# Performance work log

Measured on AMD Instinct MI355X. Metric: run time of the kernel, lower is better.

The kernel has to match this reference:

```python
import jax, jax.numpy as jnp
import numpy as np

LN2 = float(np.log(2.0))
N_ATOMS = 100_000
N_PAIRS = 2_000_000
F = 64     # number_of_atom_features
R = 16     # number_of_radial_basis_functions
N_RES = 3


def setup_inputs() -> dict:
    key = jax.random.key(0)
    ks = jax.random.split(key, 16)
    s = 0.05
    inp = {
        "pair_indices": jax.random.randint(ks[0], (2, N_PAIRS), 0, N_ATOMS, dtype=jnp.int32),
        "f_ij": jax.random.normal(ks[1], (N_PAIRS, 1, R), dtype=jnp.float32),
        "d_ij": jax.random.uniform(ks[2], (N_PAIRS, 1), dtype=jnp.float32),
        "atomic_embedding": jax.random.normal(ks[3], (N_ATOMS, F), dtype=jnp.float32),
        # AttentionMask parameter G: [F, R]
        "G": jax.random.normal(ks[4], (F, R), dtype=jnp.float32),
        # interaction_i / interaction_j linear layers (stored as [in, out])
        "Wi": jax.random.normal(ks[5], (F, F), dtype=jnp.float32) * s,
        "bi": jnp.zeros((F,), dtype=jnp.float32),
        "Wj": jax.random.normal(ks[6], (F, F), dtype=jnp.float32) * s,
        "bj": jnp.zeros((F,), dtype=jnp.float32),
        # residual blocks, stacked over N_RES
        "res_W1": jax.random.normal(ks[7], (N_RES, F, F), dtype=jnp.float32) * s,
        "res_b1": jnp.zeros((N_RES, F), dtype=jnp.float32),
        "res_W2": jax.random.normal(ks[8], (N_RES, F, F), dtype=jnp.float32) * s,
        "res_b2": jnp.zeros((N_RES, F), dtype=jnp.float32),
        # process_v linear
        "Wv": jax.random.normal(ks[9], (F, F), dtype=jnp.float32) * s,
        "bv": jnp.zeros((F,), dtype=jnp.float32),
    }
    return inp


def reference(pair_indices, f_ij, d_ij, atomic_embedding,
              G, Wi, bi, Wj, bj, res_W1, res_b1, res_W2, res_b2, Wv, bv):
    idx_i, idx_j = pair_indices[0], pair_indices[1]
    f = f_ij.squeeze(1)                                  # [P, R]

    # ShiftedSoftplus on node embeddings
    x = jax.nn.softplus(atomic_embedding) - LN2          # [N, F]

    x_i_prime = jax.nn.softplus(x @ Wi + bi)             # [N, F]
    x_j_prime = jax.nn.softplus(x[idx_j] @ Wj + bj)      # [P, F] (gather)
    f_prime = f @ G.T                                    # [P, F] attention mask

    msg = x_j_prime * f_prime                            # [P, F]
    summed = jax.ops.segment_sum(msg, idx_i, num_segments=atomic_embedding.shape[0])

    v = x_i_prime + summed                               # [N, F]
    for l in range(res_W1.shape[0]):
        h = jax.nn.softplus(v @ res_W1[l] + res_b1[l])
        v = v + (h @ res_W2[l] + res_b2[l])
    return jax.nn.softplus(v) @ Wv + bv
```

## Files before the change

### kernel.cpp

```cpp
#include <hip/hip_runtime.h>
#include <math.h>

#define FDIM 64
#define RDIM 16
#define LN2F 0.69314718055994530942f
#define LTS 68
#define NBINR 14336
#define NCHUNK 64

typedef __bf16 bf8_t __attribute__((ext_vector_type(8)));
typedef float  f4_t  __attribute__((ext_vector_type(4)));
typedef _Float16 h2_t __attribute__((ext_vector_type(2)));

__device__ __forceinline__ float sp(float x) {
    return fmaxf(x, 0.0f) + __logf(1.0f + __expf(-fabsf(x)));
}

__device__ __forceinline__ float fdot2f(h2_t a, h2_t b, float c) {
#if __has_builtin(__builtin_amdgcn_fdot2)
    return __builtin_amdgcn_fdot2(a, b, c, false);
#else
    return c + (float)a[0] * (float)b[0] + (float)a[1] * (float)b[1];
#endif
}

__global__ __launch_bounds__(256) void k_prep(
    const float* s0, const float* s1, const float* s2, const float* s3,
    const float* s4, const float* s5, const float* s6, const float* s7,
    const float* s8, __bf16* __restrict__ dst)
{
    const float* srcs[9] = {s0, s1, s2, s3, s4, s5, s6, s7, s8};
    const float* W = srcs[blockIdx.x];
    __bf16* d = dst + (size_t)blockIdx.x * 4096;
    for (int slot = threadIdx.x; slot < 512; slot += 256) {
        int f = slot >> 6, l = slot & 63;
        int kt = f >> 2, nt = f & 3;
        int row0 = kt * 32 + (l >> 4) * 8;
        int col = nt * 16 + (l & 15);
#pragma unroll
        for (int j = 0; j < 8; ++j)
            d[slot * 8 + j] = (__bf16)W[(row0 + j) * FDIM + col];
    }
}

__global__ __launch_bounds__(256) void k_hist2(
    const int* __restrict__ idx_i, int* __restrict__ Cmat,
    int P, int N, int nRange)
{
    __shared__ int h[NBINR];
    const int chunk = blockIdx.x / nRange;
    const int range = blockIdx.x % nRange;
    const int lo = range * NBINR;
    const int nb = min(NBINR, N - lo);
    for (int u = threadIdx.x; u < NBINR; u += 256) h[u] = 0;
    __syncthreads();

    const int chunkSz = (P + NCHUNK - 1) / NCHUNK;
    const int cs = chunk * chunkSz;
    const int ce = min(P, cs + chunkSz);
    int p = cs + threadIdx.x;
    for (; p + 768 < ce; p += 1024) {
        int i0 = idx_i[p];
        int i1 = idx_i[p + 256];
        int i2 = idx_i[p + 512];
        int i3 = idx_i[p + 768];
        unsigned u0 = (unsigned)(i0 - lo);
        unsigned u1 = (unsigned)(i1 - lo);
        unsigned u2 = (unsigned)(i2 - lo);
        unsigned u3 = (unsigned)(i3 - lo);
        if (u0 < (unsigned)nb) atomicAdd(&h[u0], 1);
        if (u1 < (unsigned)nb) atomicAdd(&h[u1], 1);
        if (u2 < (unsigned)nb) atomicAdd(&h[u2], 1);
        if (u3 < (unsigned)nb) atomicAdd(&h[u3], 1);
    }
    for (; p < ce; p += 256) {
        unsigned u = (unsigned)(idx_i[p] - lo);
        if (u < (unsigned)nb) atomicAdd(&h[u], 1);
    }
    __syncthreads();
    for (int u = threadIdx.x; u < nb; u += 256)
        Cmat[(size_t)chunk * N + lo + u] = h[u];
}

__global__ __launch_bounds__(256) void k_scanR(
    int* __restrict__ Cmat, int* __restrict__ tot, int N)
{
    const int bA = blockIdx.x * 512 + threadIdx.x;
    const int bB = bA + 256;
    const bool okA = bA < N, okB = bB < N;
    int runA = 0, runB = 0;
    for (int c = 0; c < NCHUNK; ++c) {
        const size_t base = (size_t)c * N;
        if (okA) { int val = Cmat[base + bA]; Cmat[base + bA] = runA; runA += val; }
        if (okB) { int val = Cmat[base + bB]; Cmat[base + bB] = runB; runB += val; }
    }
    if (okA) tot[bA] = runA;
    if (okB) tot[bB] = runB;
}

__device__ __forceinline__ void tile_in(float* T, const float* __restrict__ src,
                                        int a0, int rows, int lane)
{
#pragma unroll 4
    for (int i = 0; i < 16; ++i) {
        int r = i * 4 + (lane >> 4);
        int col = (lane & 15) * 4;
        float4 val = make_float4(0.f, 0.f, 0.f, 0.f);
        if (r < rows) val = *(const float4*)&src[(size_t)(a0 + r) * FDIM + col];
        *(float4*)&T[r * LTS + col] = val;
    }
}

__device__ __forceinline__ void build_a(const float* T, int lane, bool actLn2,
                                        bf8_t (&aF)[4][2])
{
    const int l15 = lane & 15, quad = lane >> 4;
#pragma unroll
    for (int mt = 0; mt < 4; ++mt) {
#pragma unroll
        for (int kt = 0; kt < 2; ++kt) {
            const float* rp = &T[(mt * 16 + l15) * LTS + kt * 32 + quad * 8];
            float4 u0 = *(const float4*)rp;
            float4 u1 = *(const float4*)(rp + 4);
            float e[8] = {u0.x, u0.y, u0.z, u0.w, u1.x, u1.y, u1.z, u1.w};
            bf8_t f;
#pragma unroll
            for (int j = 0; j < 8; ++j) {
                float t = actLn2 ? (sp(e[j]) - LN2F) : e[j];
                f[j] = (__bf16)t;
            }
            aF[mt][kt] = f;
        }
    }
}

__global__ __launch_bounds__(256) void k_atoms(
    const float* __restrict__ emb, const __bf16* __restrict__ wf,
    const float* __restrict__ bi, const float* __restrict__ bj,
    float* __restrict__ v, float* __restrict__ y, int N)
{
    __shared__ float tile[4][64 * LTS];
    const int lane = threadIdx.x & 63;
    const int wv = threadIdx.x >> 6;
    float* T = tile[wv];
    const int l15 = lane & 15, quad = lane >> 4;

    const bf8_t* wiF = (const bf8_t*)wf;
    const bf8_t* wjF = (const bf8_t*)(wf + 4096);
    bf8_t wi[2][4], wj[2][4];
#pragma unroll
    for (int kt = 0; kt < 2; ++kt)
#pragma unroll
        for (int nt = 0; nt < 4; ++nt) {
            wi[kt][nt] = wiF[(kt * 4 + nt) * 64 + lane];
            wj[kt][nt] = wjF[(kt * 4 + nt) * 64 + lane];
        }
    float biv[4], bjv[4];
#pragma unroll
    for (int nt = 0; nt < 4; ++nt) {
        biv[nt] = bi[nt * 16 + l15];
        bjv[nt] = bj[nt * 16 + l15];
    }

    const int nTiles = (N + 63) >> 6;
    for (int t = blockIdx.x * 4 + wv; t < nTiles; t += gridDim.x * 4) {
        const int a0 = t << 6;
        const int rows = min(64, N - a0);
        tile_in(T, emb, a0, rows, lane);
        bf8_t aF[4][2];
        build_a(T, lane, true, aF);
#pragma unroll
        for (int mt = 0; mt < 4; ++mt)
#pragma unroll
            for (int nt = 0; nt < 4; ++nt) {
                f4_t acc = {biv[nt], biv[nt], biv[nt], biv[nt]};
                acc = __builtin_amdgcn_mfma_f32_16x16x32_bf16(aF[mt][0], wi[0][nt], acc, 0, 0, 0);
                acc = __builtin_amdgcn_mfma_f32_16x16x32_bf16(aF[mt][1], wi[1][nt], acc, 0, 0, 0);
#pragma unroll
                for (int reg = 0; reg < 4; ++reg) {
                    int r = mt * 16 + quad * 4 + reg;
                    if (r < rows) v[(size_t)(a0 + r) * FDIM + nt * 16 + l15] = sp(acc[reg]);
                }
            }
#pragma unroll
        for (int mt = 0; mt < 4; ++mt)
#pragma unroll
            for (int nt = 0; nt < 4; ++nt) {
                f4_t acc = {bjv[nt], bjv[nt], bjv[nt], bjv[nt]};
                acc = __builtin_amdgcn_mfma_f32_16x16x32_bf16(aF[mt][0], wj[0][nt], acc, 0, 0, 0);
                acc = __builtin_amdgcn_mfma_f32_16x16x32_bf16(aF[mt][1], wj[1][nt], acc, 0, 0, 0);
#pragma unroll
                for (int reg = 0; reg < 4; ++reg) {
                    int r = mt * 16 + quad * 4 + reg;
                    if (r < rows) y[(size_t)(a0 + r) * FDIM + nt * 16 + l15] = sp(acc[reg]);
                }
            }
    }
}

__global__ __launch_bounds__(256) void k_post(
    const __bf16* __restrict__ wf,
    const float* __restrict__ rb1, const float* __restrict__ rb2,
    const float* __restrict__ bv,
    float* __restrict__ v, int N)
{
    __shared__ float tile[4][64 * LTS];
    const int lane = threadIdx.x & 63;
    const int wv = threadIdx.x >> 6;
    float* T = tile[wv];
    const int l15 = lane & 15, quad = lane >> 4;

    float b1v[3][4], b2v[3][4], bvv[4];
#pragma unroll
    for (int l = 0; l < 3; ++l)
#pragma unroll
        for (int nt = 0; nt < 4; ++nt) {
            b1v[l][nt] = rb1[l * FDIM + nt * 16 + l15];
            b2v[l][nt] = rb2[l * FDIM + nt * 16 + l15];
        }
#pragma unroll
    for (int nt = 0; nt < 4; ++nt) bvv[nt] = bv[nt * 16 + l15];

    const int nTiles = (N + 63) >> 6;
    for (int t = blockIdx.x * 4 + wv; t < nTiles; t += gridDim.x * 4) {
        const int a0 = t << 6;
        const int rows = min(64, N - a0);
        tile_in(T, v, a0, rows, lane);
        float vC[16][4];
#pragma unroll
        for (int mt = 0; mt < 4; ++mt)
#pragma unroll
            for (int nt = 0; nt < 4; ++nt)
#pragma unroll
                for (int reg = 0; reg < 4; ++reg)
                    vC[mt * 4 + nt][reg] =
                        T[(mt * 16 + quad * 4 + reg) * LTS + nt * 16 + l15];

        for (int l = 0; l < 3; ++l) {
            const bf8_t* w1f = (const bf8_t*)(wf + (size_t)(2 * l) * 4096);
            const bf8_t* w2f = (const bf8_t*)(wf + (size_t)(2 * l + 1) * 4096);
            bf8_t aF[4][2];
            build_a(T, lane, false, aF);
#pragma unroll
            for (int mt = 0; mt < 4; ++mt)
#pragma unroll
                for (int nt = 0; nt < 4; ++nt) {
                    f4_t acc = {b1v[l][nt], b1v[l][nt], b1v[l][nt], b1v[l][nt]};
                    acc = __builtin_amdgcn_mfma_f32_16x16x32_bf16(aF[mt][0], w1f[(0 * 4 + nt) * 64 + lane], acc, 0, 0, 0);
                    acc = __builtin_amdgcn_mfma_f32_16x16x32_bf16(aF[mt][1], w1f[(1 * 4 + nt) * 64 + lane], acc, 0, 0, 0);
#pragma unroll
                    for (int reg = 0; reg < 4; ++reg)
                        T[(mt * 16 + quad * 4 + reg) * LTS + nt * 16 + l15] = sp(acc[reg]);
                }
            bf8_t hF[4][2];
            build_a(T, lane, false, hF);
#pragma unroll
            for (int mt = 0; mt < 4; ++mt)
#pragma unroll
                for (int nt = 0; nt < 4; ++nt) {
                    f4_t acc = {b2v[l][nt], b2v[l][nt], b2v[l][nt], b2v[l][nt]};
                    acc = __builtin_amdgcn_mfma_f32_16x16x32_bf16(hF[mt][0], w2f[(0 * 4 + nt) * 64 + lane], acc, 0, 0, 0);
                    acc = __builtin_amdgcn_mfma_f32_16x16x32_bf16(hF[mt][1], w2f[(1 * 4 + nt) * 64 + lane], acc, 0, 0, 0);
#pragma unroll
                    for (int reg = 0; reg < 4; ++reg)
                        vC[mt * 4 + nt][reg] += acc[reg];
                }
            if (l < 2) {
#pragma unroll
                for (int mt = 0; mt < 4; ++mt)
#pragma unroll
                    for (int nt = 0; nt < 4; ++nt)
#pragma unroll
                        for (int reg = 0; reg < 4; ++reg)
                            T[(mt * 16 + quad * 4 + reg) * LTS + nt * 16 + l15] =
                                vC[mt * 4 + nt][reg];
            }
        }
#pragma unroll
        for (int mt = 0; mt < 4; ++mt)
#pragma unroll
            for (int nt = 0; nt < 4; ++nt)
#pragma unroll
                for (int reg = 0; reg < 4; ++reg)
                    T[(mt * 16 + quad * 4 + reg) * LTS + nt * 16 + l15] =
                        sp(vC[mt * 4 + nt][reg]);
        bf8_t fF[4][2];
        build_a(T, lane, false, fF);
        const bf8_t* wvf = (const bf8_t*)(wf + (size_t)6 * 4096);
#pragma unroll
        for (int mt = 0; mt < 4; ++mt)
#pragma unroll
            for (int nt = 0; nt < 4; ++nt) {
                f4_t acc = {bvv[nt], bvv[nt], bvv[nt], bvv[nt]};
                acc = __builtin_amdgcn_mfma_f32_16x16x32_bf16(fF[mt][0], wvf[(0 * 4 + nt) * 64 + lane], acc, 0, 0, 0);
                acc = __builtin_amdgcn_mfma_f32_16x16x32_bf16(fF[mt][1], wvf[(1 * 4 + nt) * 64 + lane], acc, 0, 0, 0);
#pragma unroll
                for (int reg = 0; reg < 4; ++reg) {
                    int r = mt * 16 + quad * 4 + reg;
                    if (r < rows) v[(size_t)(a0 + r) * FDIM + nt * 16 + l15] = acc[reg];
                }
            }
    }
}

__global__ __launch_bounds__(256) void k_scan_a(
    const int* __restrict__ cnt, int* __restrict__ part, int N)
{
    __shared__ int red[256];
    int b = blockIdx.x, t = threadIdx.x;
    int base = b * 1024 + t * 4;
    int s = 0;
#pragma unroll
    for (int i = 0; i < 4; ++i) { int a = base + i; if (a < N) s += cnt[a]; }
    red[t] = s; __syncthreads();
    for (int off = 128; off > 0; off >>= 1) {
        if (t < off) red[t] += red[t + off];
        __syncthreads();
    }
    if (t == 0) part[b] = red[0];
}

__global__ __launch_bounds__(256) void k_scan_b(int* __restrict__ part, int nPart)
{
    __shared__ int lds[256];
    int t = threadIdx.x;
    int base = t * 4;
    int v[4]; int s = 0;
#pragma unroll
    for (int i = 0; i < 4; ++i) { v[i] = (base + i < nPart) ? part[base + i] : 0; s += v[i]; }
    lds[t] = s; __syncthreads();
    int run = s;
    for (int off = 1; off < 256; off <<= 1) {
        int x = (t >= off) ? lds[t - off] : 0;
        __syncthreads();
        lds[t] += x;
        __syncthreads();
    }
    int excl = lds[t] - run;
#pragma unroll
    for (int i = 0; i < 4; ++i) { if (base + i < nPart) { part[base + i] = excl; excl += v[i]; } }
}

__global__ __launch_bounds__(256) void k_scan_c(
    const int* __restrict__ cnt, const int* __restrict__ part,
    int* __restrict__ start, int N, int P)
{
    __shared__ int lds[256];
    int b = blockIdx.x, t = threadIdx.x;
    int base = b * 1024 + t * 4;
    int v[4]; int s = 0;
#pragma unroll
    for (int i = 0; i < 4; ++i) { int a = base + i; v[i] = (a < N) ? cnt[a] : 0; s += v[i]; }
    lds[t] = s; __syncthreads();
    int run = s;
    for (int off = 1; off < 256; off <<= 1) {
        int x = (t >= off) ? lds[t - off] : 0;
        __syncthreads();
        lds[t] += x;
        __syncthreads();
    }
    int pre = part[b] + (lds[t] - run);
#pragma unroll
    for (int i = 0; i < 4; ++i) {
        int a = base + i;
        if (a < N) { start[a] = pre; pre += v[i]; }
    }
    if (b == 0 && t == 0) start[N] = P;
}

__global__ __launch_bounds__(256) void k_scatter2(
    const int* __restrict__ pidx, const float* __restrict__ f_ij,
    const int* __restrict__ Cmat, const int* __restrict__ start,
    int* __restrict__ sortedJ, _Float16* __restrict__ sortedF,
    int P, int N, int nRange)
{
    __shared__ int cur[NBINR];
    const int chunk = blockIdx.x / nRange;
    const int range = blockIdx.x % nRange;
    const int lo = range * NBINR;
    const int nb = min(NBINR, N - lo);
    for (int u = threadIdx.x; u < nb; u += 256)
        cur[u] = start[lo + u] + Cmat[(size_t)chunk * N + lo + u];
    __syncthreads();

    const int chunkSz = (P + NCHUNK - 1) / NCHUNK;
    const int cs = chunk * chunkSz;
    const int ce = min(P, cs + chunkSz);
    for (int p = cs + threadIdx.x; p < ce; p += 256) {
        int i = pidx[p];
        unsigned u = (unsigned)(i - lo);
        if (u < (unsigned)nb) {
            int j = pidx[P + p];
            int pos = atomicAdd(&cur[u], 1);
            sortedJ[pos] = j;
            const float4* fp = (const float4*)(f_ij + (size_t)p * RDIM);
            float4 A = fp[0], B = fp[1], C4 = fp[2], D = fp[3];
            h2_t hv[8];
            hv[0] = h2_t{(_Float16)A.x, (_Float16)A.y};
            hv[1] = h2_t{(_Float16)A.z, (_Float16)A.w};
            hv[2] = h2_t{(_Float16)B.x, (_Float16)B.y};
            hv[3] = h2_t{(_Float16)B.z, (_Float16)B.w};
            hv[4] = h2_t{(_Float16)C4.x, (_Float16)C4.y};
            hv[5] = h2_t{(_Float16)C4.z, (_Float16)C4.w};
            hv[6] = h2_t{(_Float16)D.x, (_Float16)D.y};
            hv[7] = h2_t{(_Float16)D.z, (_Float16)D.w};
            _Float16* dst = sortedF + (size_t)pos * 16;
            *(uint4*)dst = *(const uint4*)&hv[0];
            *(uint4*)(dst + 8) = *(const uint4*)&hv[4];
        }
    }
}

__global__ __launch_bounds__(256) void k_seg(
    const int* __restrict__ sortedJ, const _Float16* __restrict__ sortedF,
    const int* __restrict__ start, const float* __restrict__ G,
    const float* __restrict__ y, float* __restrict__ v, int N)
{
    const int c = threadIdx.x & 63;
    const int w = __builtin_amdgcn_readfirstlane((blockIdx.x << 2) | (threadIdx.x >> 6));
    const int nw = gridDim.x << 2;

    h2_t g2[8];
    {
        const float4* gp = (const float4*)(G + c * RDIM);
        float4 g0 = gp[0], g1 = gp[1], g2v = gp[2], g3 = gp[3];
        g2[0] = h2_t{(_Float16)g0.x, (_Float16)g0.y};
        g2[1] = h2_t{(_Float16)g0.z, (_Float16)g0.w};
        g2[2] = h2_t{(_Float16)g1.x, (_Float16)g1.y};
        g2[3] = h2_t{(_Float16)g1.z, (_Float16)g1.w};
        g2[4] = h2_t{(_Float16)g2v.x, (_Float16)g2v.y};
        g2[5] = h2_t{(_Float16)g2v.z, (_Float16)g2v.w};
        g2[6] = h2_t{(_Float16)g3.x, (_Float16)g3.y};
        g2[7] = h2_t{(_Float16)g3.z, (_Float16)g3.w};
    }

    for (int a = w; a < N; a += nw) {
        const int s = __builtin_amdgcn_readfirstlane(start[a]);
        const int e = __builtin_amdgcn_readfirstlane(start[a + 1]);
        float vold = v[(size_t)a * FDIM + c];
        float acc0 = 0.f, acc1 = 0.f, acc2 = 0.f, acc3 = 0.f;

        for (int base = s; base < e; base += 64) {
            const int nn = (e - base < 64) ? (e - base) : 64;
            const int li = (c < nn) ? c : (nn - 1);
            const int jkv = sortedJ[base + li];

            int k = 0;
            for (; k + 8 <= nn; k += 8) {
                int jj[8];
#pragma unroll
                for (int u = 0; u < 8; ++u)
                    jj[u] = __builtin_amdgcn_readlane(jkv, k + u);
                float yv[8];
#pragma unroll
                for (int u = 0; u < 8; ++u)
                    yv[u] = y[(size_t)jj[u] * FDIM + c];
                const h2_t* f2 = (const h2_t*)(sortedF + (size_t)(base + k) * 16);
#pragma unroll
                for (int u = 0; u < 8; ++u) {
                    float d = 0.f;
#pragma unroll
                    for (int r = 0; r < 8; ++r)
                        d = fdot2f(f2[u * 8 + r], g2[r], d);
                    if ((u & 3) == 0) acc0 = fmaf(d, yv[u], acc0);
                    else if ((u & 3) == 1) acc1 = fmaf(d, yv[u], acc1);
                    else if ((u & 3) == 2) acc2 = fmaf(d, yv[u], acc2);
                    else acc3 = fmaf(d, yv[u], acc3);
                }
            }
            for (; k < nn; ++k) {
                const int j0 = __builtin_amdgcn_readlane(jkv, k);
                float y0 = y[(size_t)j0 * FDIM + c];
                const h2_t* f2 = (const h2_t*)(sortedF + (size_t)(base + k) * 16);
                float d = 0.f;
#pragma unroll
                for (int r = 0; r < 8; ++r)
                    d = fdot2f(f2[r], g2[r], d);
                acc0 = fmaf(d, y0, acc0);
            }
        }

        v[(size_t)a * FDIM + c] = vold + (acc0 + acc1) + (acc2 + acc3);
    }
}

extern "C" void kernel_launch(void* const* d_in, const int* in_sizes, int n_in,
                              void* d_out, int out_size, void* d_ws, size_t ws_size,
                              hipStream_t stream)
{
    const int*   pidx = (const int*)d_in[0];
    const float* f_ij = (const float*)d_in[1];
    const float* emb  = (const float*)d_in[3];
    const float* G    = (const float*)d_in[4];
    const float* Wi   = (const float*)d_in[5];
    const float* bi   = (const float*)d_in[6];
    const float* Wj   = (const float*)d_in[7];
    const float* bj   = (const float*)d_in[8];
    const float* rW1  = (const float*)d_in[9];
    const float* rb1  = (const float*)d_in[10];
    const float* rW2  = (const float*)d_in[11];
    const float* rb2  = (const float*)d_in[12];
    const float* Wv   = (const float*)d_in[13];
    const float* bv   = (const float*)d_in[14];

    const int P = in_sizes[0] / 2;
    const int N = in_sizes[3] / FDIM;

    float* v = (float*)d_out;

    char* ws = (char*)d_ws;
    size_t off = 0;
    float*  y      = (float*)(ws + off);
    int*    Cmat   = (int*)(ws + off);    off += (size_t)N * FDIM * 4;
    int*    tot    = (int*)(ws + off);    off += (size_t)N * 4;
    int*    start  = (int*)(ws + off);    off += (size_t)(N + 1) * 4;
    off = (off + 15) & ~(size_t)15;
    int*    part   = (int*)(ws + off);    off += (size_t)4096 * 4;
    off = (off + 15) & ~(size_t)15;
    int*    sortedJ = (int*)(ws + off);   off += (size_t)P * 4;
    off = (off + 63) & ~(size_t)63;
    _Float16* sortedF = (_Float16*)(ws + off); off += (size_t)P * 16 * 2;
    off = (off + 15) & ~(size_t)15;
    __bf16* wf     = (__bf16*)(ws + off); off += (size_t)9 * 4096 * 2;

    const int nRange = (N + NBINR - 1) / NBINR;
    const int nPart = (N + 1023) / 1024;
    const int nTiles = (N + 63) >> 6;
    const int gTiles = (nTiles + 3) / 4;

    dim3 blk(256);
    k_prep<<<9, blk, 0, stream>>>(Wi, Wj, rW1, rW2, rW1 + 4096, rW2 + 4096,
                                  rW1 + 8192, rW2 + 8192, Wv, wf);
    k_hist2<<<NCHUNK * nRange, blk, 0, stream>>>(pidx, Cmat, P, N, nRange);
    k_scanR<<<(N + 511) / 512, blk, 0, stream>>>(Cmat, tot, N);
    k_scan_a<<<nPart, blk, 0, stream>>>(tot, part, N);
    k_scan_b<<<1, blk, 0, stream>>>(part, nPart);
    k_scan_c<<<nPart, blk, 0, stream>>>(tot, part, start, N, P);
    k_scatter2<<<NCHUNK * nRange, blk, 0, stream>>>(pidx, f_ij, Cmat, start,
                                                    sortedJ, sortedF, P, N, nRange);
    k_atoms<<<gTiles, blk, 0, stream>>>(emb, wf, bi, bj, v, y, N);
    k_seg<<<4096, blk, 0, stream>>>(sortedJ, sortedF, start, G, y, v, N);
    k_post<<<gTiles, blk, 0, stream>>>(wf + (size_t)2 * 4096, rb1, rb2, bv, v, N);
}
```

Baseline: 711.9 us.

## Split scatter into index-only scatter plus separate f_ij gather kernel

The scatter kernel now writes only (pair index, j) pairs to a sorted int2 buffer, with a 4x unrolled loop for more loads in flight. A new kernel then reads that buffer in order, gathers the f_ij rows, converts them to fp16 and writes sortedJ/sortedF contiguously. Before, each of the nRange blocks per chunk scanned all pairs but only loaded f_ij for its own range, giving scattered 64-byte reads and writes inside an atomic-heavy loop. The change adds an extra kernel launch and an extra P*8-byte buffer written and read back, and the f_ij reads are now random gathers.

```diff
diff --git a/kernel.cpp b/kernel.cpp
--- a/kernel.cpp
+++ b/kernel.cpp
@@ -22,6 +22,22 @@
 #else
     return c + (float)a[0] * (float)b[0] + (float)a[1] * (float)b[1];
 #endif
+}
+
+__device__ __forceinline__ void cvt_store16(_Float16* dst, float4 A, float4 B,
+                                            float4 C4, float4 D)
+{
+    h2_t hv[8];
+    hv[0] = h2_t{(_Float16)A.x,  (_Float16)A.y};
+    hv[1] = h2_t{(_Float16)A.z,  (_Float16)A.w};
+    hv[2] = h2_t{(_Float16)B.x,  (_Float16)B.y};
+    hv[3] = h2_t{(_Float16)B.z,  (_Float16)B.w};
+    hv[4] = h2_t{(_Float16)C4.x, (_Float16)C4.y};
+    hv[5] = h2_t{(_Float16)C4.z, (_Float16)C4.w};
+    hv[6] = h2_t{(_Float16)D.x,  (_Float16)D.y};
+    hv[7] = h2_t{(_Float16)D.z,  (_Float16)D.w};
+    *(uint4*)dst       = *(const uint4*)&hv[0];
+    *(uint4*)(dst + 8) = *(const uint4*)&hv[4];
 }
 
 __global__ __launch_bounds__(256) void k_prep(
@@ -369,9 +385,8 @@
 }
 
 __global__ __launch_bounds__(256) void k_scatter2(
-    const int* __restrict__ pidx, const float* __restrict__ f_ij,
-    const int* __restrict__ Cmat, const int* __restrict__ start,
-    int* __restrict__ sortedJ, _Float16* __restrict__ sortedF,
+    const int* __restrict__ pidx, const int* __restrict__ Cmat,
+    const int* __restrict__ start, int2* __restrict__ sorted,
     int P, int N, int nRange)
 {
     __shared__ int cur[NBINR];
@@ -386,28 +401,71 @@
     const int chunkSz = (P + NCHUNK - 1) / NCHUNK;
     const int cs = chunk * chunkSz;
     const int ce = min(P, cs + chunkSz);
-    for (int p = cs + threadIdx.x; p < ce; p += 256) {
+    int p = cs + threadIdx.x;
+    for (; p + 768 < ce; p += 1024) {
+        int i0 = pidx[p];
+        int i1 = pidx[p + 256];
+        int i2 = pidx[p + 512];
+        int i3 = pidx[p + 768];
+        int j0 = pidx[P + p];
+        int j1 = pidx[P + p + 256];
+        int j2 = pidx[P + p + 512];
+        int j3 = pidx[P + p + 768];
+        unsigned u0 = (unsigned)(i0 - lo);
+        unsigned u1 = (unsigned)(i1 - lo);
+        unsigned u2 = (unsigned)(i2 - lo);
+        unsigned u3 = (unsigned)(i3 - lo);
+        if (u0 < (unsigned)nb) { int pos = atomicAdd(&cur[u0], 1); sorted[pos] = make_int2(p, j0); }
+        if (u1 < (unsigned)nb) { int pos = atomicAdd(&cur[u1], 1); sorted[pos] = make_int2(p + 256, j1); }
+        if (u2 < (unsigned)nb) { int pos = atomicAdd(&cur[u2], 1); sorted[pos] = make_int2(p + 512, j2); }
+        if (u3 < (unsigned)nb) { int pos = atomicAdd(&cur[u3], 1); sorted[pos] = make_int2(p + 768, j3); }
+    }
+    for (; p < ce; p += 256) {
         int i = pidx[p];
         unsigned u = (unsigned)(i - lo);
         if (u < (unsigned)nb) {
             int j = pidx[P + p];
             int pos = atomicAdd(&cur[u], 1);
-            sortedJ[pos] = j;
-            const float4* fp = (const float4*)(f_ij + (size_t)p * RDIM);
-            float4 A = fp[0], B = fp[1], C4 = fp[2], D = fp[3];
-            h2_t hv[8];
-            hv[0] = h2_t{(_Float16)A.x, (_Float16)A.y};
-            hv[1] = h2_t{(_Float16)A.z, (_Float16)A.w};
-            hv[2] = h2_t{(_Float16)B.x, (_Float16)B.y};
-            hv[3] = h2_t{(_Float16)B.z, (_Float16)B.w};
-            hv[4] = h2_t{(_Float16)C4.x, (_Float16)C4.y};
-            hv[5] = h2_t{(_Float16)C4.z, (_Float16)C4.w};
-            hv[6] = h2_t{(_Float16)D.x, (_Float16)D.y};
-            hv[7] = h2_t{(_Float16)D.z, (_Float16)D.w};
-            _Float16* dst = sortedF + (size_t)pos * 16;
-            *(uint4*)dst = *(const uint4*)&hv[0];
-            *(uint4*)(dst + 8) = *(const uint4*)&hv[4];
+            sorted[pos] = make_int2(p, j);
         }
+    }
+}
+
+__global__ __launch_bounds__(256) void k_gatherF(
+    const int2* __restrict__ sorted, const float* __restrict__ f_ij,
+    int* __restrict__ sortedJ, _Float16* __restrict__ sortedF, int P)
+{
+    int t = blockIdx.x * blockDim.x + threadIdx.x;
+    int n = gridDim.x * blockDim.x;
+    int pos = t;
+    for (; pos + 3 * n < P; pos += 4 * n) {
+        int2 E0 = sorted[pos];
+        int2 E1 = sorted[pos + n];
+        int2 E2 = sorted[pos + 2 * n];
+        int2 E3 = sorted[pos + 3 * n];
+        const float4* f0 = (const float4*)(f_ij + (size_t)E0.x * RDIM);
+        const float4* f1 = (const float4*)(f_ij + (size_t)E1.x * RDIM);
+        const float4* f2 = (const float4*)(f_ij + (size_t)E2.x * RDIM);
+        const float4* f3 = (const float4*)(f_ij + (size_t)E3.x * RDIM);
+        float4 a0 = f0[0], b0 = f0[1], c0 = f0[2], d0 = f0[3];
+        float4 a1 = f1[0], b1 = f1[1], c1 = f1[2], d1 = f1[3];
+        float4 a2 = f2[0], b2 = f2[1], c2 = f2[2], d2 = f2[3];
+        float4 a3 = f3[0], b3 = f3[1], c3 = f3[2], d3 = f3[3];
+        sortedJ[pos]         = E0.y;
+        sortedJ[pos + n]     = E1.y;
+        sortedJ[pos + 2 * n] = E2.y;
+        sortedJ[pos + 3 * n] = E3.y;
+        cvt_store16(sortedF + (size_t)pos * 16,           a0, b0, c0, d0);
+        cvt_store16(sortedF + (size_t)(pos + n) * 16,     a1, b1, c1, d1);
+        cvt_store16(sortedF + (size_t)(pos + 2 * n) * 16, a2, b2, c2, d2);
+        cvt_store16(sortedF + (size_t)(pos + 3 * n) * 16, a3, b3, c3, d3);
+    }
+    for (; pos < P; pos += n) {
+        int2 E = sorted[pos];
+        const float4* fp = (const float4*)(f_ij + (size_t)E.x * RDIM);
+        float4 A = fp[0], B = fp[1], C4 = fp[2], D = fp[3];
+        sortedJ[pos] = E.y;
+        cvt_store16(sortedF + (size_t)pos * 16, A, B, C4, D);
     }
 }
 
@@ -517,6 +575,8 @@
     off = (off + 15) & ~(size_t)15;
     int*    part   = (int*)(ws + off);    off += (size_t)4096 * 4;
     off = (off + 15) & ~(size_t)15;
+    int2*   sorted = (int2*)(ws + off);   off += (size_t)P * 8;
+    off = (off + 15) & ~(size_t)15;
     int*    sortedJ = (int*)(ws + off);   off += (size_t)P * 4;
     off = (off + 63) & ~(size_t)63;
     _Float16* sortedF = (_Float16*)(ws + off); off += (size_t)P * 16 * 2;
@@ -536,8 +596,8 @@
     k_scan_a<<<nPart, blk, 0, stream>>>(tot, part, N);
     k_scan_b<<<1, blk, 0, stream>>>(part, nPart);
     k_scan_c<<<nPart, blk, 0, stream>>>(tot, part, start, N, P);
-    k_scatter2<<<NCHUNK * nRange, blk, 0, stream>>>(pidx, f_ij, Cmat, start,
-                                                    sortedJ, sortedF, P, N, nRange);
+    k_scatter2<<<NCHUNK * nRange, blk, 0, stream>>>(pidx, Cmat, start, sorted, P, N, nRange);
+    k_gatherF<<<2048, blk, 0, stream>>>(sorted, f_ij, sortedJ, sortedF, P);
     k_atoms<<<gTiles, blk, 0, stream>>>(emb, wf, bi, bj, v, y, N);
     k_seg<<<4096, blk, 0, stream>>>(sortedJ, sortedF, start, G, y, v, N);
     k_post<<<gTiles, blk, 0, stream>>>(wf + (size_t)2 * 4096, rb1, rb2, bv, v, N);
```

New measurement: 635.6 us. 10.7% less time.
